# Performance work log

Hardware: AMD Instinct MI355X
Metric: run time of the kernel (lower is better)

Reference implementation:

```python
import jax, jax.numpy as jnp
import numpy as np
from jax import lax

WS = 5      # window_size
NH = 8      # num_heads
C = 192     # channels
CPH = (2 * C // 3) // (2 * NH)  # per-head channel dim = 8


def _l2n(x):
    # F.normalize(dim=-1) with eps clamp
    n = jnp.linalg.norm(x, axis=-1, keepdims=True)
    return x / jnp.maximum(n, 1e-12)


def _conv3(x, w, b):
    y = lax.conv_general_dilated(x, w, (1, 1), 'SAME',
                                 dimension_numbers=('NCHW', 'OIHW', 'NCHW'))
    return y + b[None, :, None, None]


def _cpb_bias(cpb_w1, cpb_b1, cpb_w2):
    # relative coords table, Swin-V2 style log-spaced
    rel = np.arange(-(WS - 1), WS, dtype=np.float32)
    tbl = np.stack(np.meshgrid(rel, rel, indexing='ij'), axis=-1)  # (2W-1,2W-1,2)
    tbl = tbl / (WS - 1) * 8.0
    tbl = np.sign(tbl) * np.log2(np.abs(tbl) + 1.0) / np.log2(8.0)
    tbl = jnp.asarray(tbl.reshape(-1, 2))                          # (81,2)
    # relative position index (static int table)
    coords = np.stack(np.meshgrid(np.arange(WS), np.arange(WS), indexing='ij')).reshape(2, -1)
    rc = (coords[:, :, None] - coords[:, None, :]).transpose(1, 2, 0)  # (25,25,2)
    rc[..., 0] += WS - 1
    rc[..., 1] += WS - 1
    rc[..., 0] *= 2 * WS - 1
    idx = rc.sum(-1).reshape(-1)                                    # (625,)
    # cpb MLP: Linear(2,512)+ReLU, Linear(512,NH,no bias)
    h = jax.nn.relu(tbl @ cpb_w1.T + cpb_b1)
    bias_tbl = h @ cpb_w2.T                                         # (81, NH)
    bias = bias_tbl[idx].reshape(WS * WS, WS * WS, NH).transpose(2, 0, 1)
    return 16.0 * jax.nn.sigmoid(bias)                              # (NH,25,25)


def _wa(x, logit_scale, bias):
    # windowed cosine attention; note: scores are K@K^T (faithful to source)
    b, c2, h, w = x.shape
    hb, wb = h // WS, w // WS
    # 'b (kv head c) (h dh) (w dw) -> kv (b h w) head (dh dw) c'
    xr = x.reshape(b, 2, NH, CPH, hb, WS, wb, WS)
    xr = xr.transpose(1, 0, 4, 6, 2, 5, 7, 3).reshape(2, b * hb * wb, NH, WS * WS, CPH)
    k, v = xr[0], xr[1]
    kn = _l2n(k)
    scale = jnp.exp(jnp.minimum(logit_scale, jnp.log(100.0)))       # (NH,1,1)
    atn = jnp.einsum('wnic,wnjc->wnij', kn, kn) * scale + bias[None]
    atn = jax.nn.softmax(atn, axis=-1)
    y = jnp.einsum('wnij,wnjc->wnic', atn, v)                       # (bhw,NH,25,CPH)
    y = y.reshape(b, hb, wb, NH, WS, WS, CPH)
    y = y.transpose(0, 3, 6, 1, 4, 2, 5).reshape(b, NH * CPH, h, w)
    return y


def _forward(x, w_in, b_in, w_out, b_out, logit_scale, lr_logit_scale,
             cpb_w1, cpb_b1, cpb_w2):
    b, c, h, w = x.shape
    xp = _conv3(x, w_in, b_in)                                      # (b, 2c, h, w)
    ch = 2 * c // 3
    x0, x1, x2 = xp[:, :ch], xp[:, ch:2 * ch], xp[:, 2 * ch:]
    bias = _cpb_bias(cpb_w1, cpb_b1, cpb_w2)
    ys = []
    # branch 0: plain window attention
    ys.append(_wa(x0, logit_scale, bias))
    # branch 1: shifted windows (note asymmetric shifts, faithful to torch code)
    x1s = jnp.roll(x1, shift=(-WS // 2, -WS // 2), axis=(2, 3))
    y1 = _wa(x1s, logit_scale, bias)
    y1 = jnp.roll(y1, shift=(WS // 2, WS // 2), axis=(2, 3))
    ys.append(y1)
    # branch 2: long-range axial cosine attention
    xr = x2.reshape(b, 2, NH, CPH, h, w).transpose(1, 0, 4, 2, 5, 3)
    xr = xr.reshape(2, b * h, NH, w, CPH)                           # kv,(b h),head,w,c
    k, v = xr[0], xr[1]
    scale = jnp.exp(jnp.minimum(lr_logit_scale, jnp.log(100.0)))
    kn = _l2n(k)
    atn = jax.nn.softmax(jnp.einsum('bnic,bnjc->bnij', kn, kn) * scale, axis=-1)
    v = jnp.einsum('bnij,bnjc->bnic', atn, v)
    # '(b h) head w c -> (b w) head h c'
    k = k.reshape(b, h, NH, w, CPH).transpose(0, 3, 2, 1, 4).reshape(b * w, NH, h, CPH)
    v = v.reshape(b, h, NH, w, CPH).transpose(0, 3, 2, 1, 4).reshape(b * w, NH, h, CPH)
    kn = _l2n(k)
    atn = jax.nn.softmax(jnp.einsum('bnic,bnjc->bnij', kn, kn) * scale, axis=-1)
    v = jnp.einsum('bnij,bnjc->bnic', atn, v)
    # '(b w) head h c -> b (head c) h w'
    y2 = v.reshape(b, w, NH, h, CPH).transpose(0, 2, 4, 3, 1).reshape(b, NH * CPH, h, w)
    ys.append(y2)
    y = jnp.concatenate(ys, axis=1)                                 # (b, c, h, w)
    return _conv3(y, w_out, b_out)


def setup_inputs() -> dict:
    key = jax.random.key(0)
    ks = jax.random.split(key, 8)
    B, H, W = 2, 160, 160
    s = 0.02
    return {
        'x': jax.random.normal(ks[0], (B, C, H, W), jnp.float32),
        'w_in': jax.random.normal(ks[1], (2 * C, C, 3, 3), jnp.float32) * s,
        'b_in': jnp.zeros((2 * C,), jnp.float32),
        'w_out': jax.random.normal(ks[2], (C, C, 3, 3), jnp.float32) * s,
        'b_out': jnp.zeros((C,), jnp.float32),
        'logit_scale': jnp.log(10.0 * jnp.ones((NH, 1, 1), jnp.float32)),
        'lr_logit_scale': jnp.log(10.0 * jnp.ones((NH, 1, 1), jnp.float32)),
        'cpb_w1': jax.random.normal(ks[3], (512, 2), jnp.float32) * s,
        'cpb_b1': jnp.zeros((512,), jnp.float32),
        'cpb_w2': jax.random.normal(ks[4], (NH, 512), jnp.float32) * s,
    }


def reference(x, w_in, b_in, w_out, b_out, logit_scale, lr_logit_scale,
              cpb_w1, cpb_b1, cpb_w2):
    return _forward(x, w_in, b_in, w_out, b_out, logit_scale, lr_logit_scale,
                    cpb_w1, cpb_b1, cpb_w2)
```

## Files before the change

kernel.cpp:

```cpp
#include <hip/hip_runtime.h>
#include <math.h>


typedef __attribute__((ext_vector_type(8))) short short8;
typedef __attribute__((ext_vector_type(4))) short short4v;
typedef __attribute__((ext_vector_type(4))) float f32x4;

constexpr int Hc = 160, Wc = 160, Bc = 2;
constexpr int HPR = 162;
constexpr int HPW = 164;

__device__ inline unsigned short f2bf(float f) {
  union { float f; unsigned u; } v; v.f = f;
  unsigned r = v.u + 0x7FFF + ((v.u >> 16) & 1);
  return (unsigned short)(r >> 16);
}
__device__ inline float bf2f(unsigned short h) {
  union { unsigned u; float f; } v; v.u = ((unsigned)h) << 16;
  return v.f;
}

__device__ inline void gl16(const void* g, void* l) {
  __builtin_amdgcn_global_load_lds((const __attribute__((address_space(1))) unsigned int*)g,
                                   (__attribute__((address_space(3))) unsigned int*)l, 16, 0, 0);
}

__device__ inline float dot8(f32x4 a0, f32x4 a1, f32x4 b0, f32x4 b1) {
  float d = a0[0] * b0[0];
  d = fmaf(a0[1], b0[1], d); d = fmaf(a0[2], b0[2], d); d = fmaf(a0[3], b0[3], d);
  d = fmaf(a1[0], b1[0], d); d = fmaf(a1[1], b1[1], d);
  d = fmaf(a1[2], b1[2], d); d = fmaf(a1[3], b1[3], d);
  return d;
}

__global__ __launch_bounds__(256)
void zero_borders(unsigned short* __restrict__ xpad, unsigned short* __restrict__ ypad) {
  const int NPOS = 968;
  const int total = 2 * 2 * NPOS * 24;
  int idx = blockIdx.x * 256 + threadIdx.x;
  if (idx >= total) return;
  const int ch = idx % 24; int q = idx / 24;
  const int pos = q % NPOS; q /= NPOS;
  const int b = q & 1; const int buf = q >> 1;
  int row, col;
  if (pos < 328) { row = (pos < 164) ? 0 : 161; col = pos % 164; }
  else { int r = pos - 328; row = 1 + (r >> 2); int cm = r & 3; col = cm == 0 ? 0 : 160 + cm; }
  unsigned short* p = (buf ? ypad : xpad) + (((size_t)b * HPR + row) * HPW + col) * 192 + ch * 8;
  short8 z = {};
  *(short8*)p = z;
}

__global__ __launch_bounds__(256)
void nchw2nhwc_pad(const float* __restrict__ x, unsigned short* __restrict__ xpad) {
  __shared__ float tile[192][33];
  int blk = blockIdx.x;
  const int w0 = (blk % 5) * 32; blk /= 5;
  const int h = blk % 160;
  const int b = blk / 160;
  const int t = threadIdx.x;
  for (int i = t; i < 192 * 32; i += 256) {
    int c = i >> 5, w = i & 31;
    tile[c][w] = x[(((size_t)b * 192 + c) * 160 + h) * 160 + w0 + w];
  }
  __syncthreads();
  for (int i = t; i < 32 * 192; i += 256) {
    int w = i / 192, c = i % 192;
    xpad[(((size_t)b * HPR + h + 1) * HPW + w0 + w + 1) * 192 + c] = f2bf(tile[c][w]);
  }
}

__global__ __launch_bounds__(256)
void wtransformA(const float* __restrict__ w, unsigned short* __restrict__ wtr, int CO, int CI) {
  int id = blockIdx.x * 256 + threadIdx.x;
  if (id >= CO * CI) return;
  const int co = id / CI, ci = id % CI;
  const int cs = ci >> 5, kh = (ci >> 3) & 3, j = ci & 7;
  const int cotile = co >> 4, cor = co & 15;
  const int NT = CO / 16;
  const float* wp = w + (size_t)id * 9;
#pragma unroll
  for (int tap = 0; tap < 9; ++tap)
    wtr[((((size_t)tap * 6 + cs) * NT + cotile) * 64 + kh * 16 + cor) * 8 + j] = f2bf(wp[tap]);
}

template<int COUT, int OUTMODE>
__global__ __launch_bounds__(256, 2)
void conv_mfma(const unsigned short* __restrict__ xin, const unsigned short* __restrict__ wtrA,
               const float* __restrict__ bias, unsigned short* __restrict__ obf,
               float* __restrict__ of32) {
  constexpr int CIN = 192;
  constexpr int BH = 4, R = 6;
  constexpr int TOTAL = R * 84 * 4;
  constexpr int SLAB = R * 84 * 32;
  constexpr int NT = COUT / 16;
  __shared__ unsigned short slab[2 * SLAB];
  const int t = threadIdx.x, lane = t & 63, wid = t >> 6;
  const int bx = blockIdx.x, cog = blockIdx.y, b = blockIdx.z;
  const int ws = bx & 1, hb = bx >> 1;
  const int w0 = ws * 80, h0 = hb * BH;
  const int hr = wid;
  const int l15 = lane & 15, l4 = lane >> 4;
  const int co0 = cog * 64;

  f32x4 acc[5][4];
#pragma unroll
  for (int ct = 0; ct < 4; ++ct) {
    f32x4 bi;
#pragma unroll
    for (int r = 0; r < 4; ++r) bi[r] = bias[co0 + ct * 16 + l4 * 4 + r];
#pragma unroll
    for (int mt = 0; mt < 5; ++mt) acc[mt][ct] = bi;
  }

  auto stage = [&](int cs, int bufbase) {
#pragma unroll
    for (int ib0 = 0; ib0 < 8; ++ib0) {
      const int ib = ib0 * 4 + wid;
      const int n = ib * 64 + lane;
      if (n < TOTAL) {
        const int c = n & 3, q = n >> 2;
        const int r = q / 84, wv = q - r * 84;
        const int csrc = c ^ ((wv >> 1) & 3);
        const unsigned short* g = xin +
            (((size_t)b * HPR + h0 + r) * HPW + w0 + wv) * CIN + cs * 32 + csrc * 8;
        gl16(g, &slab[bufbase + ib * 512]);
      }
    }
  };

#define LOADA(a, ky, cs)                                                         \
  {                                                                              \
    _Pragma("unroll")                                                            \
    for (int kx = 0; kx < 3; ++kx) {                                             \
      _Pragma("unroll")                                                          \
      for (int ct = 0; ct < 4; ++ct)                                             \
        a[kx * 4 + ct] = *(const short8*)(wtrA +                                 \
            ((size_t)(((ky) * 3 + kx) * 6 + (cs)) * NT + cog * 4 + ct) * 512 +   \
            lane * 8);                                                           \
    }                                                                            \
  }

#define GROUP(a, ky, bufbase)                                                    \
  {                                                                              \
    const unsigned short* srow = &slab[(bufbase) + (hr + (ky)) * 84 * 32];       \
    _Pragma("unroll")                                                            \
    for (int kx = 0; kx < 3; ++kx) {                                             \
      _Pragma("unroll")                                                          \
      for (int mt = 0; mt < 5; ++mt) {                                           \
        const int wv = mt * 16 + l15 + kx;                                       \
        const int cr = l4 ^ ((wv >> 1) & 3);                                     \
        short8 bf = *(const short8*)(srow + wv * 32 + cr * 8);                   \
        _Pragma("unroll")                                                        \
        for (int ct = 0; ct < 4; ++ct)                                           \
          acc[mt][ct] =                                                          \
              __builtin_amdgcn_mfma_f32_16x16x32_bf16(a[kx * 4 + ct], bf,        \
                                                      acc[mt][ct], 0, 0, 0);     \
      }                                                                          \
    }                                                                            \
  }

#define CSBODY(P, Q, cs, base, nbase)                                            \
  {                                                                              \
    if ((cs) < 5) stage((cs) + 1, nbase);                                        \
    LOADA(Q, 1, cs);                                                             \
    GROUP(P, 0, base);                                                           \
    LOADA(P, 2, cs);                                                             \
    GROUP(Q, 1, base);                                                           \
    if ((cs) < 5) LOADA(Q, 0, (cs) + 1);                                         \
    GROUP(P, 2, base);                                                           \
    __syncthreads();                                                             \
  }

  short8 Pf[12], Qf[12];
  stage(0, 0);
  LOADA(Pf, 0, 0);
  __syncthreads();

  CSBODY(Pf, Qf, 0, 0, SLAB);
  CSBODY(Qf, Pf, 1, SLAB, 0);
  CSBODY(Pf, Qf, 2, 0, SLAB);
  CSBODY(Qf, Pf, 3, SLAB, 0);
  CSBODY(Pf, Qf, 4, 0, SLAB);
  CSBODY(Qf, Pf, 5, SLAB, 0);
#undef LOADA
#undef GROUP
#undef CSBODY

  const int h = h0 + hr;
  if (OUTMODE == 0) {
#pragma unroll
    for (int mt = 0; mt < 5; ++mt) {
      const int w = w0 + mt * 16 + l15;
      unsigned short* dst0 = obf + (((size_t)b * Hc + h) * Wc + w) * 384 + co0 + l4 * 4;
#pragma unroll
      for (int ct = 0; ct < 4; ++ct) {
        short4v s;
#pragma unroll
        for (int r = 0; r < 4; ++r) s[r] = (short)f2bf(acc[mt][ct][r]);
        *(short4v*)(dst0 + ct * 16) = s;
      }
    }
  } else {
#pragma unroll
    for (int mt = 0; mt < 5; ++mt) {
      const int w = w0 + mt * 16 + l15;
#pragma unroll
      for (int ct = 0; ct < 4; ++ct)
#pragma unroll
        for (int r = 0; r < 4; ++r) {
          const int co = co0 + ct * 16 + l4 * 4 + r;
          of32[(((size_t)b * COUT + co) * Hc + h) * Wc + w] = acc[mt][ct][r];
        }
    }
  }
}

__global__ __launch_bounds__(64)
void cpb_bias_kernel(const float* __restrict__ w1, const float* __restrict__ b1,
                     const float* __restrict__ w2, float* __restrict__ biasf) {
  const int e = blockIdx.x;
  const int d0 = e / 9, d1 = e % 9;
  const int r0 = d0 - 4, r1 = d1 - 4;
  float t0 = log2f(fabsf((float)r0) * 2.0f + 1.0f) * (1.0f / 3.0f); if (r0 < 0) t0 = -t0;
  float t1 = log2f(fabsf((float)r1) * 2.0f + 1.0f) * (1.0f / 3.0f); if (r1 < 0) t1 = -t1;
  const int lane = threadIdx.x;
  float acc[8];
#pragma unroll
  for (int n = 0; n < 8; ++n) acc[n] = 0.f;
  for (int k = lane; k < 512; k += 64) {
    float hk = fmaf(t0, w1[k * 2 + 0], fmaf(t1, w1[k * 2 + 1], b1[k]));
    hk = fmaxf(hk, 0.f);
#pragma unroll
    for (int n = 0; n < 8; ++n) acc[n] = fmaf(hk, w2[n * 512 + k], acc[n]);
  }
#pragma unroll
  for (int n = 0; n < 8; ++n) {
#pragma unroll
    for (int off = 32; off > 0; off >>= 1) acc[n] += __shfl_xor(acc[n], off, 64);
  }
  if (lane == 0) {
#pragma unroll
    for (int n = 0; n < 8; ++n)
      biasf[e * 8 + n] = 16.0f / (1.0f + expf(-acc[n]));
  }
}

__global__ __launch_bounds__(256)
void win_attn_kernel(const unsigned short* __restrict__ xq, const float* __restrict__ biasf,
                     const float* __restrict__ logit_scale, unsigned short* __restrict__ ypad) {
  __shared__ f32x4 kn4[8][25][2];
  __shared__ f32x4 vv4[8][25][2];
  const int head = threadIdx.x >> 5;
  const int i = threadIdx.x & 31;
  const int variant = blockIdx.y;
  const int chan_off = variant ? 128 : 0;
  const int y_ch_off = variant ? 64 : 0;
  const int shift_in = variant ? 3 : 0;
  const int shift_out = variant ? 2 : 0;
  int blk = blockIdx.x;
  const int wb_i = blk % 32; blk /= 32;
  const int hb_i = blk;
  const int b = blockIdx.z;
  const int wi = i / 5, wj = i % 5;
  const int gh = hb_i * 5 + wi, gw = wb_i * 5 + wj;
  const int sh = (gh + shift_in) % Hc, sw = (gw + shift_in) % Wc;

  if (i < 25) {
    const unsigned short* base = xq + (((size_t)b * Hc + sh) * Wc + sw) * 384 + chan_off + head * 8;
    short8 kv = *(const short8*)base;
    short8 vv = *(const short8*)(base + 64);
    float k[8]; float nrm = 0.f;
#pragma unroll
    for (int c = 0; c < 8; ++c) { k[c] = bf2f((unsigned short)kv[c]); nrm = fmaf(k[c], k[c], nrm); }
    const float inv = 1.0f / fmaxf(sqrtf(nrm), 1e-12f);
    f32x4 a0, a1, b0, b1;
#pragma unroll
    for (int c = 0; c < 4; ++c) { a0[c] = k[c] * inv; a1[c] = k[c + 4] * inv; }
#pragma unroll
    for (int c = 0; c < 4; ++c) { b0[c] = bf2f((unsigned short)vv[c]); b1[c] = bf2f((unsigned short)vv[c + 4]); }
    kn4[head][i][0] = a0; kn4[head][i][1] = a1;
    vv4[head][i][0] = b0; vv4[head][i][1] = b1;
  }
  __syncthreads();
  if (i >= 25) return;

  const float scale = expf(fminf(logit_scale[head], 4.6051702f));
  const f32x4 q0 = kn4[head][i][0], q1 = kn4[head][i][1];
  float s[25];
#pragma unroll
  for (int j = 0; j < 25; ++j) {
    const float d = dot8(q0, q1, kn4[head][j][0], kn4[head][j][1]);
    const int d0 = wi - (j / 5) + 4, d1 = wj - (j % 5) + 4;
    s[j] = fmaf(d, scale, biasf[(d0 * 9 + d1) * 8 + head]);
  }
  float m = -1e30f;
#pragma unroll
  for (int j = 0; j < 25; ++j) m = fmaxf(m, s[j]);
  float den = 0.f;
  f32x4 acc0 = {0.f, 0.f, 0.f, 0.f}, acc1 = {0.f, 0.f, 0.f, 0.f};
#pragma unroll
  for (int j = 0; j < 25; ++j) {
    const float p = __expf(s[j] - m);
    den += p;
    acc0 += vv4[head][j][0] * p;
    acc1 += vv4[head][j][1] * p;
  }
  const float rden = 1.0f / den;
  const int oh = (gh + shift_out) % Hc, ow = (gw + shift_out) % Wc;
  short8 o;
#pragma unroll
  for (int c = 0; c < 4; ++c) { o[c] = (short)f2bf(acc0[c] * rden); o[c + 4] = (short)f2bf(acc1[c] * rden); }
  *(short8*)(ypad + (((size_t)b * HPR + oh + 1) * HPW + ow + 1) * 192 + y_ch_off + head * 8) = o;
}

__global__ __launch_bounds__(192)
void row_attn_kernel(const unsigned short* __restrict__ xq, const float* __restrict__ lrs,
                     unsigned short* __restrict__ vrow) {
  __shared__ f32x4 kn4[160][2];
  __shared__ f32x4 vv4[160][2];
  int blk = blockIdx.x;
  const int head = blk % 8; blk /= 8;
  const int h = blk % 160; blk /= 160;
  const int b = blk;
  const int i = threadIdx.x;

  if (i < 160) {
    const unsigned short* base = xq + (((size_t)b * Hc + h) * Wc + i) * 384 + 256 + head * 8;
    short8 kv = *(const short8*)base;
    short8 vv = *(const short8*)(base + 64);
    float k[8]; float nrm = 0.f;
#pragma unroll
    for (int c = 0; c < 8; ++c) { k[c] = bf2f((unsigned short)kv[c]); nrm = fmaf(k[c], k[c], nrm); }
    const float inv = 1.0f / fmaxf(sqrtf(nrm), 1e-12f);
    f32x4 a0, a1, b0, b1;
#pragma unroll
    for (int c = 0; c < 4; ++c) { a0[c] = k[c] * inv; a1[c] = k[c + 4] * inv; }
#pragma unroll
    for (int c = 0; c < 4; ++c) { b0[c] = bf2f((unsigned short)vv[c]); b1[c] = bf2f((unsigned short)vv[c + 4]); }
    kn4[i][0] = a0; kn4[i][1] = a1;
    vv4[i][0] = b0; vv4[i][1] = b1;
  }
  __syncthreads();
  if (i >= 160) return;

  const float scale = expf(fminf(lrs[head], 4.6051702f));
  const f32x4 q0 = kn4[i][0], q1 = kn4[i][1];
  float den = 0.f;
  f32x4 acc0 = {0.f, 0.f, 0.f, 0.f}, acc1 = {0.f, 0.f, 0.f, 0.f};
  for (int j = 0; j < 160; ++j) {
    const float d = dot8(q0, q1, kn4[j][0], kn4[j][1]);
    const float p = __expf(fmaf(d, scale, -scale));
    den += p;
    acc0 += vv4[j][0] * p;
    acc1 += vv4[j][1] * p;
  }
  const float rden = 1.0f / den;
  short8 o;
#pragma unroll
  for (int c = 0; c < 4; ++c) { o[c] = (short)f2bf(acc0[c] * rden); o[c + 4] = (short)f2bf(acc1[c] * rden); }
  *(short8*)(vrow + ((((size_t)b * 8 + head) * 160 + h) * 160 + i) * 8) = o;
}

__global__ __launch_bounds__(192)
void col_attn_kernel(const unsigned short* __restrict__ xq, const float* __restrict__ lrs,
                     const unsigned short* __restrict__ vrow, unsigned short* __restrict__ ypad) {
  __shared__ f32x4 kn4[160][2];
  __shared__ f32x4 vv4[160][2];
  int blk = blockIdx.x;
  const int head = blk % 8; blk /= 8;
  const int w = blk % 160; blk /= 160;
  const int b = blk;
  const int i = threadIdx.x;

  if (i < 160) {
    const unsigned short* kb = xq + (((size_t)b * Hc + i) * Wc + w) * 384 + 256 + head * 8;
    short8 kv = *(const short8*)kb;
    short8 vv = *(const short8*)(vrow + ((((size_t)b * 8 + head) * 160 + i) * 160 + w) * 8);
    float k[8]; float nrm = 0.f;
#pragma unroll
    for (int c = 0; c < 8; ++c) { k[c] = bf2f((unsigned short)kv[c]); nrm = fmaf(k[c], k[c], nrm); }
    const float inv = 1.0f / fmaxf(sqrtf(nrm), 1e-12f);
    f32x4 a0, a1, b0, b1;
#pragma unroll
    for (int c = 0; c < 4; ++c) { a0[c] = k[c] * inv; a1[c] = k[c + 4] * inv; }
#pragma unroll
    for (int c = 0; c < 4; ++c) { b0[c] = bf2f((unsigned short)vv[c]); b1[c] = bf2f((unsigned short)vv[c + 4]); }
    kn4[i][0] = a0; kn4[i][1] = a1;
    vv4[i][0] = b0; vv4[i][1] = b1;
  }
  __syncthreads();
  if (i >= 160) return;

  const float scale = expf(fminf(lrs[head], 4.6051702f));
  const f32x4 q0 = kn4[i][0], q1 = kn4[i][1];
  float den = 0.f;
  f32x4 acc0 = {0.f, 0.f, 0.f, 0.f}, acc1 = {0.f, 0.f, 0.f, 0.f};
  for (int j = 0; j < 160; ++j) {
    const float d = dot8(q0, q1, kn4[j][0], kn4[j][1]);
    const float p = __expf(fmaf(d, scale, -scale));
    den += p;
    acc0 += vv4[j][0] * p;
    acc1 += vv4[j][1] * p;
  }
  const float rden = 1.0f / den;
  short8 o;
#pragma unroll
  for (int c = 0; c < 4; ++c) { o[c] = (short)f2bf(acc0[c] * rden); o[c + 4] = (short)f2bf(acc1[c] * rden); }
  *(short8*)(ypad + (((size_t)b * HPR + i + 1) * HPW + w + 1) * 192 + 128 + head * 8) = o;
}

extern "C" void kernel_launch(void* const* d_in, const int* in_sizes, int n_in,
                              void* d_out, int out_size, void* d_ws, size_t ws_size,
                              hipStream_t stream) {
  const float* x     = (const float*)d_in[0];
  const float* w_in  = (const float*)d_in[1];
  const float* b_in  = (const float*)d_in[2];
  const float* w_out = (const float*)d_in[3];
  const float* b_out = (const float*)d_in[4];
  const float* ls    = (const float*)d_in[5];
  const float* lrs   = (const float*)d_in[6];
  const float* cw1   = (const float*)d_in[7];
  const float* cb1   = (const float*)d_in[8];
  const float* cw2   = (const float*)d_in[9];
  float* out = (float*)d_out;

  char* p = (char*)d_ws;
  unsigned short* xpad = (unsigned short*)p;  p += (size_t)Bc * HPR * HPW * 192 * 2;
  unsigned short* ypad = (unsigned short*)p;  p += (size_t)Bc * HPR * HPW * 192 * 2;
  unsigned short* xq   = (unsigned short*)p;  p += (size_t)Bc * Hc * Wc * 384 * 2;
  unsigned short* vrow = (unsigned short*)p;  p += (size_t)Bc * 8 * Hc * Wc * 8 * 2;
  unsigned short* wtr1 = (unsigned short*)p;  p += (size_t)9 * 384 * 192 * 2;
  unsigned short* wtr2 = (unsigned short*)p;  p += (size_t)9 * 192 * 192 * 2;
  float* biasf = (float*)p;

  zero_borders<<<(2 * 2 * 968 * 24 + 255) / 256, 256, 0, stream>>>(xpad, ypad);
  nchw2nhwc_pad<<<Bc * 160 * 5, 256, 0, stream>>>(x, xpad);
  wtransformA<<<(384 * 192 + 255) / 256, 256, 0, stream>>>(w_in, wtr1, 384, 192);
  wtransformA<<<(192 * 192 + 255) / 256, 256, 0, stream>>>(w_out, wtr2, 192, 192);
  cpb_bias_kernel<<<81, 64, 0, stream>>>(cw1, cb1, cw2, biasf);
  conv_mfma<384, 0><<<dim3(80, 6, Bc), 256, 0, stream>>>(xpad, wtr1, b_in, xq, nullptr);
  win_attn_kernel<<<dim3(1024, 2, Bc), 256, 0, stream>>>(xq, biasf, ls, ypad);
  row_attn_kernel<<<Bc * 160 * 8, 192, 0, stream>>>(xq, lrs, vrow);
  col_attn_kernel<<<Bc * 160 * 8, 192, 0, stream>>>(xq, lrs, vrow, ypad);
  conv_mfma<192, 1><<<dim3(80, 3, Bc), 256, 0, stream>>>(ypad, wtr2, b_out, nullptr, out);
}
```

Measured before the change: 267.8 us.

## Merge prep and attention kernels, deepen conv A-fragment prefetch with raw barriers

Five preprocessing launches (pad/transpose, border zeroing, two weight transforms, CPB bias) become one kernel that branches on block index. Windowed attention and row attention share a single launch, which cuts launch overhead and lets both run at once. The conv main loop now holds three A-fragment register sets prefetched a full channel slice ahead, uses s_setprio around MFMA groups, and replaces __syncthreads with a partial vmcnt wait plus s_barrier. The risks are higher register pressure and a hand-tuned vmcnt(36) that must match the actual number of outstanding loads.

```diff
diff --git a/kernel.cpp b/kernel.cpp
--- a/kernel.cpp
+++ b/kernel.cpp
@@ -34,53 +34,86 @@
 }
 
 __global__ __launch_bounds__(256)
-void zero_borders(unsigned short* __restrict__ xpad, unsigned short* __restrict__ ypad) {
-  const int NPOS = 968;
-  const int total = 2 * 2 * NPOS * 24;
-  int idx = blockIdx.x * 256 + threadIdx.x;
-  if (idx >= total) return;
-  const int ch = idx % 24; int q = idx / 24;
-  const int pos = q % NPOS; q /= NPOS;
-  const int b = q & 1; const int buf = q >> 1;
-  int row, col;
-  if (pos < 328) { row = (pos < 164) ? 0 : 161; col = pos % 164; }
-  else { int r = pos - 328; row = 1 + (r >> 2); int cm = r & 3; col = cm == 0 ? 0 : 160 + cm; }
-  unsigned short* p = (buf ? ypad : xpad) + (((size_t)b * HPR + row) * HPW + col) * 192 + ch * 8;
-  short8 z = {};
-  *(short8*)p = z;
-}
-
-__global__ __launch_bounds__(256)
-void nchw2nhwc_pad(const float* __restrict__ x, unsigned short* __restrict__ xpad) {
+void prep_kernel(const float* __restrict__ x, unsigned short* __restrict__ xpad,
+                 unsigned short* __restrict__ ypad,
+                 const float* __restrict__ w_in, unsigned short* __restrict__ wtr1,
+                 const float* __restrict__ w_out, unsigned short* __restrict__ wtr2,
+                 const float* __restrict__ cw1, const float* __restrict__ cb1,
+                 const float* __restrict__ cw2, float* __restrict__ biasf) {
   __shared__ float tile[192][33];
-  int blk = blockIdx.x;
-  const int w0 = (blk % 5) * 32; blk /= 5;
-  const int h = blk % 160;
-  const int b = blk / 160;
+  const int bid = blockIdx.x;
   const int t = threadIdx.x;
-  for (int i = t; i < 192 * 32; i += 256) {
-    int c = i >> 5, w = i & 31;
-    tile[c][w] = x[(((size_t)b * 192 + c) * 160 + h) * 160 + w0 + w];
-  }
-  __syncthreads();
-  for (int i = t; i < 32 * 192; i += 256) {
-    int w = i / 192, c = i % 192;
-    xpad[(((size_t)b * HPR + h + 1) * HPW + w0 + w + 1) * 192 + c] = f2bf(tile[c][w]);
-  }
-}
-
-__global__ __launch_bounds__(256)
-void wtransformA(const float* __restrict__ w, unsigned short* __restrict__ wtr, int CO, int CI) {
-  int id = blockIdx.x * 256 + threadIdx.x;
-  if (id >= CO * CI) return;
-  const int co = id / CI, ci = id % CI;
-  const int cs = ci >> 5, kh = (ci >> 3) & 3, j = ci & 7;
-  const int cotile = co >> 4, cor = co & 15;
-  const int NT = CO / 16;
-  const float* wp = w + (size_t)id * 9;
-#pragma unroll
-  for (int tap = 0; tap < 9; ++tap)
-    wtr[((((size_t)tap * 6 + cs) * NT + cotile) * 64 + kh * 16 + cor) * 8 + j] = f2bf(wp[tap]);
+  if (bid < 1600) {
+    int blk = bid;
+    const int w0 = (blk % 5) * 32; blk /= 5;
+    const int h = blk % 160;
+    const int b = blk / 160;
+    for (int i = t; i < 192 * 32; i += 256) {
+      int c = i >> 5, w = i & 31;
+      tile[c][w] = x[(((size_t)b * 192 + c) * 160 + h) * 160 + w0 + w];
+    }
+    __syncthreads();
+    for (int i = t; i < 32 * 192; i += 256) {
+      int w = i / 192, c = i % 192;
+      xpad[(((size_t)b * HPR + h + 1) * HPW + w0 + w + 1) * 192 + c] = f2bf(tile[c][w]);
+    }
+  } else if (bid < 1963) {
+    const int NPOS = 968;
+    const int total = 2 * 2 * NPOS * 24;
+    int idx = (bid - 1600) * 256 + t;
+    if (idx >= total) return;
+    const int ch = idx % 24; int q = idx / 24;
+    const int pos = q % NPOS; q /= NPOS;
+    const int b = q & 1; const int buf = q >> 1;
+    int row, col;
+    if (pos < 328) { row = (pos < 164) ? 0 : 161; col = pos % 164; }
+    else { int r = pos - 328; row = 1 + (r >> 2); int cm = r & 3; col = cm == 0 ? 0 : 160 + cm; }
+    unsigned short* p = (buf ? ypad : xpad) + (((size_t)b * HPR + row) * HPW + col) * 192 + ch * 8;
+    short8 z = {};
+    *(short8*)p = z;
+  } else if (bid < 2395) {
+    const bool first = bid < 2251;
+    const int CO = first ? 384 : 192;
+    const int NT = CO / 16;
+    const float* w = first ? w_in : w_out;
+    unsigned short* wtr = first ? wtr1 : wtr2;
+    int id = (bid - (first ? 1963 : 2251)) * 256 + t;
+    if (id >= CO * 192) return;
+    const int co = id / 192, ci = id % 192;
+    const int cs = ci >> 5, kh = (ci >> 3) & 3, j = ci & 7;
+    const int cotile = co >> 4, cor = co & 15;
+    const float* wp = w + (size_t)id * 9;
+#pragma unroll
+    for (int tap = 0; tap < 9; ++tap)
+      wtr[((((size_t)tap * 6 + cs) * NT + cotile) * 64 + kh * 16 + cor) * 8 + j] = f2bf(wp[tap]);
+  } else {
+    if (t >= 64) return;
+    const int e = bid - 2395;
+    const int d0 = e / 9, d1 = e % 9;
+    const int r0 = d0 - 4, r1 = d1 - 4;
+    float t0 = log2f(fabsf((float)r0) * 2.0f + 1.0f) * (1.0f / 3.0f); if (r0 < 0) t0 = -t0;
+    float t1 = log2f(fabsf((float)r1) * 2.0f + 1.0f) * (1.0f / 3.0f); if (r1 < 0) t1 = -t1;
+    const int lane = t;
+    float acc[8];
+#pragma unroll
+    for (int n = 0; n < 8; ++n) acc[n] = 0.f;
+    for (int k = lane; k < 512; k += 64) {
+      float hk = fmaf(t0, cw1[k * 2 + 0], fmaf(t1, cw1[k * 2 + 1], cb1[k]));
+      hk = fmaxf(hk, 0.f);
+#pragma unroll
+      for (int n = 0; n < 8; ++n) acc[n] = fmaf(hk, cw2[n * 512 + k], acc[n]);
+    }
+#pragma unroll
+    for (int n = 0; n < 8; ++n) {
+#pragma unroll
+      for (int off = 32; off > 0; off >>= 1) acc[n] += __shfl_xor(acc[n], off, 64);
+    }
+    if (lane == 0) {
+#pragma unroll
+      for (int n = 0; n < 8; ++n)
+        biasf[e * 8 + n] = 16.0f / (1.0f + expf(-acc[n]));
+    }
+  }
 }
 
 template<int COUT, int OUTMODE>
@@ -89,7 +122,7 @@
                const float* __restrict__ bias, unsigned short* __restrict__ obf,
                float* __restrict__ of32) {
   constexpr int CIN = 192;
-  constexpr int BH = 4, R = 6;
+  constexpr int R = 6;
   constexpr int TOTAL = R * 84 * 4;
   constexpr int SLAB = R * 84 * 32;
   constexpr int NT = COUT / 16;
@@ -97,7 +130,7 @@
   const int t = threadIdx.x, lane = t & 63, wid = t >> 6;
   const int bx = blockIdx.x, cog = blockIdx.y, b = blockIdx.z;
   const int ws = bx & 1, hb = bx >> 1;
-  const int w0 = ws * 80, h0 = hb * BH;
+  const int w0 = ws * 80, h0 = hb * 4;
   const int hr = wid;
   const int l15 = lane & 15, l4 = lane >> 4;
   const int co0 = cog * 64;
@@ -159,29 +192,39 @@
     }                                                                            \
   }
 
-#define CSBODY(P, Q, cs, base, nbase)                                            \
+#define CSBODY(cs, base, nbase, LAST)                                            \
   {                                                                              \
-    if ((cs) < 5) stage((cs) + 1, nbase);                                        \
-    LOADA(Q, 1, cs);                                                             \
-    GROUP(P, 0, base);                                                           \
-    LOADA(P, 2, cs);                                                             \
-    GROUP(Q, 1, base);                                                           \
-    if ((cs) < 5) LOADA(Q, 0, (cs) + 1);                                         \
-    GROUP(P, 2, base);                                                           \
-    __syncthreads();                                                             \
-  }
-
-  short8 Pf[12], Qf[12];
+    if (!(LAST)) stage((cs) + 1, nbase);                                         \
+    __builtin_amdgcn_s_setprio(1);                                               \
+    GROUP(A0f, 0, base);                                                         \
+    __builtin_amdgcn_s_setprio(0);                                               \
+    if (!(LAST)) LOADA(A0f, 0, (cs) + 1);                                        \
+    __builtin_amdgcn_s_setprio(1);                                               \
+    GROUP(A1f, 1, base);                                                         \
+    __builtin_amdgcn_s_setprio(0);                                               \
+    if (!(LAST)) LOADA(A1f, 1, (cs) + 1);                                        \
+    __builtin_amdgcn_s_setprio(1);                                               \
+    GROUP(A2f, 2, base);                                                         \
+    __builtin_amdgcn_s_setprio(0);                                               \
+    if (!(LAST)) {                                                               \
+      LOADA(A2f, 2, (cs) + 1);                                                   \
+      asm volatile("s_waitcnt vmcnt(36)\n\ts_barrier" ::: "memory");             \
+    }                                                                            \
+  }
+
+  short8 A0f[12], A1f[12], A2f[12];
   stage(0, 0);
-  LOADA(Pf, 0, 0);
-  __syncthreads();
-
-  CSBODY(Pf, Qf, 0, 0, SLAB);
-  CSBODY(Qf, Pf, 1, SLAB, 0);
-  CSBODY(Pf, Qf, 2, 0, SLAB);
-  CSBODY(Qf, Pf, 3, SLAB, 0);
-  CSBODY(Pf, Qf, 4, 0, SLAB);
-  CSBODY(Qf, Pf, 5, SLAB, 0);
+  LOADA(A0f, 0, 0);
+  LOADA(A1f, 1, 0);
+  LOADA(A2f, 2, 0);
+  asm volatile("s_waitcnt vmcnt(36)\n\ts_barrier" ::: "memory");
+
+  CSBODY(0, 0, SLAB, 0);
+  CSBODY(1, SLAB, 0, 0);
+  CSBODY(2, 0, SLAB, 0);
+  CSBODY(3, SLAB, 0, 0);
+  CSBODY(4, 0, SLAB, 0);
+  CSBODY(5, SLAB, 0, 1);
 #undef LOADA
 #undef GROUP
 #undef CSBODY
@@ -215,150 +258,120 @@
   }
 }
 
-__global__ __launch_bounds__(64)
-void cpb_bias_kernel(const float* __restrict__ w1, const float* __restrict__ b1,
-                     const float* __restrict__ w2, float* __restrict__ biasf) {
-  const int e = blockIdx.x;
-  const int d0 = e / 9, d1 = e % 9;
-  const int r0 = d0 - 4, r1 = d1 - 4;
-  float t0 = log2f(fabsf((float)r0) * 2.0f + 1.0f) * (1.0f / 3.0f); if (r0 < 0) t0 = -t0;
-  float t1 = log2f(fabsf((float)r1) * 2.0f + 1.0f) * (1.0f / 3.0f); if (r1 < 0) t1 = -t1;
-  const int lane = threadIdx.x;
-  float acc[8];
-#pragma unroll
-  for (int n = 0; n < 8; ++n) acc[n] = 0.f;
-  for (int k = lane; k < 512; k += 64) {
-    float hk = fmaf(t0, w1[k * 2 + 0], fmaf(t1, w1[k * 2 + 1], b1[k]));
-    hk = fmaxf(hk, 0.f);
-#pragma unroll
-    for (int n = 0; n < 8; ++n) acc[n] = fmaf(hk, w2[n * 512 + k], acc[n]);
-  }
-#pragma unroll
-  for (int n = 0; n < 8; ++n) {
-#pragma unroll
-    for (int off = 32; off > 0; off >>= 1) acc[n] += __shfl_xor(acc[n], off, 64);
-  }
-  if (lane == 0) {
-#pragma unroll
-    for (int n = 0; n < 8; ++n)
-      biasf[e * 8 + n] = 16.0f / (1.0f + expf(-acc[n]));
-  }
-}
-
 __global__ __launch_bounds__(256)
-void win_attn_kernel(const unsigned short* __restrict__ xq, const float* __restrict__ biasf,
-                     const float* __restrict__ logit_scale, unsigned short* __restrict__ ypad) {
-  __shared__ f32x4 kn4[8][25][2];
-  __shared__ f32x4 vv4[8][25][2];
-  const int head = threadIdx.x >> 5;
-  const int i = threadIdx.x & 31;
-  const int variant = blockIdx.y;
-  const int chan_off = variant ? 128 : 0;
-  const int y_ch_off = variant ? 64 : 0;
-  const int shift_in = variant ? 3 : 0;
-  const int shift_out = variant ? 2 : 0;
-  int blk = blockIdx.x;
-  const int wb_i = blk % 32; blk /= 32;
-  const int hb_i = blk;
-  const int b = blockIdx.z;
-  const int wi = i / 5, wj = i % 5;
-  const int gh = hb_i * 5 + wi, gw = wb_i * 5 + wj;
-  const int sh = (gh + shift_in) % Hc, sw = (gw + shift_in) % Wc;
-
-  if (i < 25) {
-    const unsigned short* base = xq + (((size_t)b * Hc + sh) * Wc + sw) * 384 + chan_off + head * 8;
-    short8 kv = *(const short8*)base;
-    short8 vv = *(const short8*)(base + 64);
-    float k[8]; float nrm = 0.f;
-#pragma unroll
-    for (int c = 0; c < 8; ++c) { k[c] = bf2f((unsigned short)kv[c]); nrm = fmaf(k[c], k[c], nrm); }
-    const float inv = 1.0f / fmaxf(sqrtf(nrm), 1e-12f);
-    f32x4 a0, a1, b0, b1;
-#pragma unroll
-    for (int c = 0; c < 4; ++c) { a0[c] = k[c] * inv; a1[c] = k[c + 4] * inv; }
-#pragma unroll
-    for (int c = 0; c < 4; ++c) { b0[c] = bf2f((unsigned short)vv[c]); b1[c] = bf2f((unsigned short)vv[c + 4]); }
-    kn4[head][i][0] = a0; kn4[head][i][1] = a1;
-    vv4[head][i][0] = b0; vv4[head][i][1] = b1;
-  }
-  __syncthreads();
-  if (i >= 25) return;
-
-  const float scale = expf(fminf(logit_scale[head], 4.6051702f));
-  const f32x4 q0 = kn4[head][i][0], q1 = kn4[head][i][1];
-  float s[25];
-#pragma unroll
-  for (int j = 0; j < 25; ++j) {
-    const float d = dot8(q0, q1, kn4[head][j][0], kn4[head][j][1]);
-    const int d0 = wi - (j / 5) + 4, d1 = wj - (j % 5) + 4;
-    s[j] = fmaf(d, scale, biasf[(d0 * 9 + d1) * 8 + head]);
-  }
-  float m = -1e30f;
-#pragma unroll
-  for (int j = 0; j < 25; ++j) m = fmaxf(m, s[j]);
-  float den = 0.f;
-  f32x4 acc0 = {0.f, 0.f, 0.f, 0.f}, acc1 = {0.f, 0.f, 0.f, 0.f};
-#pragma unroll
-  for (int j = 0; j < 25; ++j) {
-    const float p = __expf(s[j] - m);
-    den += p;
-    acc0 += vv4[head][j][0] * p;
-    acc1 += vv4[head][j][1] * p;
-  }
-  const float rden = 1.0f / den;
-  const int oh = (gh + shift_out) % Hc, ow = (gw + shift_out) % Wc;
-  short8 o;
-#pragma unroll
-  for (int c = 0; c < 4; ++c) { o[c] = (short)f2bf(acc0[c] * rden); o[c + 4] = (short)f2bf(acc1[c] * rden); }
-  *(short8*)(ypad + (((size_t)b * HPR + oh + 1) * HPW + ow + 1) * 192 + y_ch_off + head * 8) = o;
-}
-
-__global__ __launch_bounds__(192)
-void row_attn_kernel(const unsigned short* __restrict__ xq, const float* __restrict__ lrs,
-                     unsigned short* __restrict__ vrow) {
-  __shared__ f32x4 kn4[160][2];
-  __shared__ f32x4 vv4[160][2];
-  int blk = blockIdx.x;
-  const int head = blk % 8; blk /= 8;
-  const int h = blk % 160; blk /= 160;
-  const int b = blk;
-  const int i = threadIdx.x;
-
-  if (i < 160) {
-    const unsigned short* base = xq + (((size_t)b * Hc + h) * Wc + i) * 384 + 256 + head * 8;
-    short8 kv = *(const short8*)base;
-    short8 vv = *(const short8*)(base + 64);
-    float k[8]; float nrm = 0.f;
-#pragma unroll
-    for (int c = 0; c < 8; ++c) { k[c] = bf2f((unsigned short)kv[c]); nrm = fmaf(k[c], k[c], nrm); }
-    const float inv = 1.0f / fmaxf(sqrtf(nrm), 1e-12f);
-    f32x4 a0, a1, b0, b1;
-#pragma unroll
-    for (int c = 0; c < 4; ++c) { a0[c] = k[c] * inv; a1[c] = k[c + 4] * inv; }
-#pragma unroll
-    for (int c = 0; c < 4; ++c) { b0[c] = bf2f((unsigned short)vv[c]); b1[c] = bf2f((unsigned short)vv[c + 4]); }
-    kn4[i][0] = a0; kn4[i][1] = a1;
-    vv4[i][0] = b0; vv4[i][1] = b1;
-  }
-  __syncthreads();
-  if (i >= 160) return;
-
-  const float scale = expf(fminf(lrs[head], 4.6051702f));
-  const f32x4 q0 = kn4[i][0], q1 = kn4[i][1];
-  float den = 0.f;
-  f32x4 acc0 = {0.f, 0.f, 0.f, 0.f}, acc1 = {0.f, 0.f, 0.f, 0.f};
-  for (int j = 0; j < 160; ++j) {
-    const float d = dot8(q0, q1, kn4[j][0], kn4[j][1]);
-    const float p = __expf(fmaf(d, scale, -scale));
-    den += p;
-    acc0 += vv4[j][0] * p;
-    acc1 += vv4[j][1] * p;
-  }
-  const float rden = 1.0f / den;
-  short8 o;
-#pragma unroll
-  for (int c = 0; c < 4; ++c) { o[c] = (short)f2bf(acc0[c] * rden); o[c + 4] = (short)f2bf(acc1[c] * rden); }
-  *(short8*)(vrow + ((((size_t)b * 8 + head) * 160 + h) * 160 + i) * 8) = o;
+void attn1_kernel(const unsigned short* __restrict__ xq, const float* __restrict__ biasf,
+                  const float* __restrict__ logit_scale, const float* __restrict__ lrs,
+                  unsigned short* __restrict__ ypad, unsigned short* __restrict__ vrow) {
+  const int bid = blockIdx.x;
+  if (bid < 4096) {
+    __shared__ f32x4 kn4[8][25][2];
+    __shared__ f32x4 vv4[8][25][2];
+    const int head = threadIdx.x >> 5;
+    const int i = threadIdx.x & 31;
+    const int b = bid >> 11;
+    const int r = bid & 2047;
+    const int variant = r >> 10;
+    const int blk = r & 1023;
+    const int chan_off = variant ? 128 : 0;
+    const int y_ch_off = variant ? 64 : 0;
+    const int shift_in = variant ? 3 : 0;
+    const int shift_out = variant ? 2 : 0;
+    const int wb_i = blk % 32, hb_i = blk / 32;
+    const int wi = i / 5, wj = i % 5;
+    const int gh = hb_i * 5 + wi, gw = wb_i * 5 + wj;
+    const int sh = (gh + shift_in) % Hc, sw = (gw + shift_in) % Wc;
+
+    if (i < 25) {
+      const unsigned short* base = xq + (((size_t)b * Hc + sh) * Wc + sw) * 384 + chan_off + head * 8;
+      short8 kv = *(const short8*)base;
+      short8 vv = *(const short8*)(base + 64);
+      float k[8]; float nrm = 0.f;
+#pragma unroll
+      for (int c = 0; c < 8; ++c) { k[c] = bf2f((unsigned short)kv[c]); nrm = fmaf(k[c], k[c], nrm); }
+      const float inv = 1.0f / fmaxf(sqrtf(nrm), 1e-12f);
+      f32x4 a0, a1, b0, b1;
+#pragma unroll
+      for (int c = 0; c < 4; ++c) { a0[c] = k[c] * inv; a1[c] = k[c + 4] * inv; }
+#pragma unroll
+      for (int c = 0; c < 4; ++c) { b0[c] = bf2f((unsigned short)vv[c]); b1[c] = bf2f((unsigned short)vv[c + 4]); }
+      kn4[head][i][0] = a0; kn4[head][i][1] = a1;
+      vv4[head][i][0] = b0; vv4[head][i][1] = b1;
+    }
+    __syncthreads();
+    if (i >= 25) return;
+
+    const float scale = expf(fminf(logit_scale[head], 4.6051702f));
+    const f32x4 q0 = kn4[head][i][0], q1 = kn4[head][i][1];
+    float s[25];
+#pragma unroll
+    for (int j = 0; j < 25; ++j) {
+      const float d = dot8(q0, q1, kn4[head][j][0], kn4[head][j][1]);
+      const int d0 = wi - (j / 5) + 4, d1 = wj - (j % 5) + 4;
+      s[j] = fmaf(d, scale, biasf[(d0 * 9 + d1) * 8 + head]);
+    }
+    float m = -1e30f;
+#pragma unroll
+    for (int j = 0; j < 25; ++j) m = fmaxf(m, s[j]);
+    float den = 0.f;
+    f32x4 acc0 = {0.f, 0.f, 0.f, 0.f}, acc1 = {0.f, 0.f, 0.f, 0.f};
+#pragma unroll
+    for (int j = 0; j < 25; ++j) {
+      const float p = __expf(s[j] - m);
+      den += p;
+      acc0 += vv4[head][j][0] * p;
+      acc1 += vv4[head][j][1] * p;
+    }
+    const float rden = 1.0f / den;
+    const int oh = (gh + shift_out) % Hc, ow = (gw + shift_out) % Wc;
+    short8 o;
+#pragma unroll
+    for (int c = 0; c < 4; ++c) { o[c] = (short)f2bf(acc0[c] * rden); o[c + 4] = (short)f2bf(acc1[c] * rden); }
+    *(short8*)(ypad + (((size_t)b * HPR + oh + 1) * HPW + ow + 1) * 192 + y_ch_off + head * 8) = o;
+  } else {
+    __shared__ f32x4 kn4[160][2];
+    __shared__ f32x4 vv4[160][2];
+    int u = bid - 4096;
+    const int head = u % 8; u /= 8;
+    const int h = u % 160;
+    const int b = u / 160;
+    const int i = threadIdx.x;
+
+    if (i < 160) {
+      const unsigned short* base = xq + (((size_t)b * Hc + h) * Wc + i) * 384 + 256 + head * 8;
+      short8 kv = *(const short8*)base;
+      short8 vv = *(const short8*)(base + 64);
+      float k[8]; float nrm = 0.f;
+#pragma unroll
+      for (int c = 0; c < 8; ++c) { k[c] = bf2f((unsigned short)kv[c]); nrm = fmaf(k[c], k[c], nrm); }
+      const float inv = 1.0f / fmaxf(sqrtf(nrm), 1e-12f);
+      f32x4 a0, a1, b0, b1;
+#pragma unroll
+      for (int c = 0; c < 4; ++c) { a0[c] = k[c] * inv; a1[c] = k[c + 4] * inv; }
+#pragma unroll
+      for (int c = 0; c < 4; ++c) { b0[c] = bf2f((unsigned short)vv[c]); b1[c] = bf2f((unsigned short)vv[c + 4]); }
+      kn4[i][0] = a0; kn4[i][1] = a1;
+      vv4[i][0] = b0; vv4[i][1] = b1;
+    }
+    __syncthreads();
+    if (i >= 160) return;
+
+    const float scale = expf(fminf(lrs[head], 4.6051702f));
+    const f32x4 q0 = kn4[i][0], q1 = kn4[i][1];
+    float den = 0.f;
+    f32x4 acc0 = {0.f, 0.f, 0.f, 0.f}, acc1 = {0.f, 0.f, 0.f, 0.f};
+    for (int j = 0; j < 160; ++j) {
+      const float d = dot8(q0, q1, kn4[j][0], kn4[j][1]);
+      const float p = __expf(fmaf(d, scale, -scale));
+      den += p;
+      acc0 += vv4[j][0] * p;
+      acc1 += vv4[j][1] * p;
+    }
+    const float rden = 1.0f / den;
+    short8 o;
+#pragma unroll
+    for (int c = 0; c < 4; ++c) { o[c] = (short)f2bf(acc0[c] * rden); o[c + 4] = (short)f2bf(acc1[c] * rden); }
+    *(short8*)(vrow + ((((size_t)b * 8 + head) * 160 + h) * 160 + i) * 8) = o;
+  }
 }
 
 __global__ __launch_bounds__(192)
@@ -433,14 +446,9 @@
   unsigned short* wtr2 = (unsigned short*)p;  p += (size_t)9 * 192 * 192 * 2;
   float* biasf = (float*)p;
 
-  zero_borders<<<(2 * 2 * 968 * 24 + 255) / 256, 256, 0, stream>>>(xpad, ypad);
-  nchw2nhwc_pad<<<Bc * 160 * 5, 256, 0, stream>>>(x, xpad);
-  wtransformA<<<(384 * 192 + 255) / 256, 256, 0, stream>>>(w_in, wtr1, 384, 192);
-  wtransformA<<<(192 * 192 + 255) / 256, 256, 0, stream>>>(w_out, wtr2, 192, 192);
-  cpb_bias_kernel<<<81, 64, 0, stream>>>(cw1, cb1, cw2, biasf);
+  prep_kernel<<<2476, 256, 0, stream>>>(x, xpad, ypad, w_in, wtr1, w_out, wtr2, cw1, cb1, cw2, biasf);
   conv_mfma<384, 0><<<dim3(80, 6, Bc), 256, 0, stream>>>(xpad, wtr1, b_in, xq, nullptr);
-  win_attn_kernel<<<dim3(1024, 2, Bc), 256, 0, stream>>>(xq, biasf, ls, ypad);
-  row_attn_kernel<<<Bc * 160 * 8, 192, 0, stream>>>(xq, lrs, vrow);
+  attn1_kernel<<<4096 + Bc * 160 * 8, 256, 0, stream>>>(xq, biasf, ls, lrs, ypad, vrow);
   col_attn_kernel<<<Bc * 160 * 8, 192, 0, stream>>>(xq, lrs, vrow, ypad);
   conv_mfma<192, 1><<<dim3(80, 3, Bc), 256, 0, stream>>>(ypad, wtr2, b_out, nullptr, out);
 }
```

Result: faster. 261.3 us (-2.4%).
